# Optimization experiments

Hardware: AMD Instinct MI355X
Metric: run time of the kernel (lower is better)

Reference implementation:

```python
import jax, jax.numpy as jnp
import numpy as np

NUM_HEADS = 8          # from init_kwargs
MASK_VALUE = -1e6      # torch code sets masked scores to -1e6 (not -inf)


def setup_inputs() -> dict:
    key = jax.random.key(0)
    k1, k2, k3, k4, k5 = jax.random.split(key, 5)
    n, S, d = 256, 512, 128   # n = B(2) * num_windows(16) * num_heads(8)
    W = 16                    # num_windows
    return {
        "queries": jax.random.normal(k1, (n, S, d), jnp.float32),
        "keys": jax.random.normal(k2, (n, S, d), jnp.float32),
        "values": jax.random.normal(k3, (n, S, d), jnp.float32),
        "valid_lens": jax.random.randint(k4, (n,), 0, S, jnp.int32),
        "window_mask": jax.random.normal(k5, (W, S, S), jnp.float32),
    }


def reference(queries, keys, values, valid_lens, window_mask):
    n, Q, d = queries.shape
    Wn, _, K = window_mask.shape
    # scaled QK^T: [n, Q, K]
    scores = jnp.einsum('bqd,bkd->bqk', queries, keys) / jnp.sqrt(
        jnp.asarray(d, queries.dtype))
    # additive window mask, broadcast over (batch, heads)
    B = n // (Wn * NUM_HEADS)
    scores = scores.reshape(B, Wn, NUM_HEADS, Q, K) + window_mask[None, :, None]
    scores = scores.reshape(n, Q, K)
    # valid-length masking: positions >= valid_lens[b] set to -1e6 before softmax
    mask = jnp.arange(K)[None, None, :] < valid_lens[:, None, None]  # [n,1,K]
    scores = jnp.where(mask, scores, MASK_VALUE)
    attn = jax.nn.softmax(scores, axis=-1)
    # dropout p=0.0 (eval) -> identity
    return jnp.einsum('bqk,bkd->bqd', attn, values)
```

## Files before the change

### kernel.cpp

```cpp
#include <hip/hip_runtime.h>

typedef unsigned short u16;
using bf16x8 = __attribute__((ext_vector_type(8))) short;
using f32x4  = __attribute__((ext_vector_type(4))) float;
using s16x4  = __attribute__((ext_vector_type(4))) short;

#define S_LEN 512
#define D_DIM 128
#define CB    32
#define KS    136
#define VS    36
#define KBUF  (CB * KS)
#define VBUF  (D_DIM * VS)
#define SCALE 0.08838834764831845f

__device__ __forceinline__ unsigned int cvt_pk_bf16(float lo, float hi) {
  unsigned int r;
  asm("v_cvt_pk_bf16_f32 %0, %1, %2" : "=v"(r) : "v"(lo), "v"(hi));
  return r;
}
__device__ __forceinline__ bf16x8 pack8(f32x4 a, f32x4 b) {
  union { unsigned int u[4]; bf16x8 v; } r;
  r.u[0] = cvt_pk_bf16(a[0], a[1]);
  r.u[1] = cvt_pk_bf16(a[2], a[3]);
  r.u[2] = cvt_pk_bf16(b[0], b[1]);
  r.u[3] = cvt_pk_bf16(b[2], b[3]);
  return r.v;
}

__global__ __launch_bounds__(256, 3)
void attn_fused(const float* __restrict__ Q, const float* __restrict__ K,
                const float* __restrict__ V, const int* __restrict__ VL,
                const float* __restrict__ WM, float* __restrict__ O) {
  __shared__ short smem[2 * KBUF + 2 * VBUF];

  const int bid  = blockIdx.x;
  const int n    = (bid & 7) | ((bid >> 6) << 3);
  const int qt   = (bid >> 3) & 7;
  const int tid  = threadIdx.x;
  const int wave = tid >> 6;
  const int L    = tid & 63;
  const int quad = L >> 4;
  const int lq   = L & 15;
  const int qw   = qt * 64 + wave * 16;
  const int qg   = qw + lq;
  const int w    = (n >> 3) & 15;

  short* Ksh = smem;
  short* VTb = smem + 2 * KBUF;

  const float* Qn  = Q + (size_t)n * S_LEN * D_DIM;
  const float* Kn  = K + (size_t)n * S_LEN * D_DIM;
  const float* Vn  = V + (size_t)n * S_LEN * D_DIM;
  const float* WMq = WM + ((size_t)w * S_LEN + qg) * S_LEN;

  const int vlen  = VL[n];
  const int kvlim = (vlen == 0) ? S_LEN : vlen;
  const int nch   = (kvlim + CB - 1) / CB;

  bf16x8 qf[4];
#pragma unroll
  for (int dc = 0; dc < 4; ++dc) {
    const f32x4* qp = (const f32x4*)(Qn + (size_t)qg * D_DIM + dc * 32 + quad * 8);
    qf[dc] = pack8(qp[0], qp[1]);
  }

  f32x4 o[8];
#pragma unroll
  for (int t = 0; t < 8; ++t) o[t] = (f32x4){0.f, 0.f, 0.f, 0.f};
  float mrun = -1e30f, lrun = 0.f;

  const int tr = tid >> 4;
  const int cc = tid & 15;
  const int colsw = (cc & 7) << 2;
  const float* Kst = Kn + (size_t)tr * D_DIM + cc * 8;
  const float* Vst = Vn + (size_t)tr * D_DIM + cc * 8;

  f32x4 k0a, k0b, k1a, k1b, v0a, v0b, v1a, v1b;

#define STAGE_ISSUE(cb_) {                                              \
    const float* kp0 = Kst + (size_t)(cb_) * D_DIM;                     \
    const float* kp1 = kp0 + 16 * D_DIM;                                \
    const float* vp0 = Vst + (size_t)(cb_) * D_DIM;                     \
    const float* vp1 = vp0 + 16 * D_DIM;                                \
    k0a = ((const f32x4*)kp0)[0]; k0b = ((const f32x4*)kp0)[1];         \
    k1a = ((const f32x4*)kp1)[0]; k1b = ((const f32x4*)kp1)[1];         \
    v0a = ((const f32x4*)vp0)[0]; v0b = ((const f32x4*)vp0)[1];         \
    v1a = ((const f32x4*)vp1)[0]; v1b = ((const f32x4*)vp1)[1]; }

#define STAGE_WRITE(kd, vd) {                                           \
    *(bf16x8*)((kd) + tr * KS + cc * 8)        = pack8(k0a, k0b);       \
    *(bf16x8*)((kd) + (16 + tr) * KS + cc * 8) = pack8(k1a, k1b);       \
    short* vt0 = (vd) + (cc * 8) * VS + (tr ^ colsw);                   \
    short* vt1 = (vd) + (cc * 8) * VS + ((16 + tr) ^ colsw);            \
    unsigned int wa0 = cvt_pk_bf16(v0a[0], v0a[1]);                     \
    unsigned int wa1 = cvt_pk_bf16(v0a[2], v0a[3]);                     \
    unsigned int wa2 = cvt_pk_bf16(v0b[0], v0b[1]);                     \
    unsigned int wa3 = cvt_pk_bf16(v0b[2], v0b[3]);                     \
    vt0[0 * VS] = (short)(wa0);  vt0[1 * VS] = (short)(wa0 >> 16);      \
    vt0[2 * VS] = (short)(wa1);  vt0[3 * VS] = (short)(wa1 >> 16);      \
    vt0[4 * VS] = (short)(wa2);  vt0[5 * VS] = (short)(wa2 >> 16);      \
    vt0[6 * VS] = (short)(wa3);  vt0[7 * VS] = (short)(wa3 >> 16);      \
    unsigned int wb0 = cvt_pk_bf16(v1a[0], v1a[1]);                     \
    unsigned int wb1 = cvt_pk_bf16(v1a[2], v1a[3]);                     \
    unsigned int wb2 = cvt_pk_bf16(v1b[0], v1b[1]);                     \
    unsigned int wb3 = cvt_pk_bf16(v1b[2], v1b[3]);                     \
    vt1[0 * VS] = (short)(wb0);  vt1[1 * VS] = (short)(wb0 >> 16);      \
    vt1[2 * VS] = (short)(wb1);  vt1[3 * VS] = (short)(wb1 >> 16);      \
    vt1[4 * VS] = (short)(wb2);  vt1[5 * VS] = (short)(wb2 >> 16);      \
    vt1[6 * VS] = (short)(wb3);  vt1[7 * VS] = (short)(wb3 >> 16); }

  STAGE_ISSUE(0);
  STAGE_WRITE(Ksh, VTb);
  asm volatile("s_waitcnt lgkmcnt(0)" ::: "memory");
  __builtin_amdgcn_s_barrier();

  int buf = 0;
  for (int ci = 0; ci < nch; ++ci) {
    const int cb   = ci * CB;
    const int cpre = (ci + 1 < nch ? ci + 1 : nch - 1) * CB;

    STAGE_ISSUE(cpre);
    f32x4 wm0 = *(const f32x4*)(WMq + cb + quad * 4);
    f32x4 wm1 = *(const f32x4*)(WMq + cb + 16 + quad * 4);
    __builtin_amdgcn_sched_barrier(0);

    const short* Kc = Ksh + buf * KBUF;
    const short* Vc = VTb + buf * VBUF;

    f32x4 a0 = {0, 0, 0, 0}, a1 = {0, 0, 0, 0};
#pragma unroll
    for (int dc = 0; dc < 4; ++dc) {
      bf16x8 kf0 = *(const bf16x8*)(Kc + lq * KS + dc * 32 + quad * 8);
      bf16x8 kf1 = *(const bf16x8*)(Kc + (16 + lq) * KS + dc * 32 + quad * 8);
      a0 = __builtin_amdgcn_mfma_f32_16x16x32_bf16(kf0, qf[dc], a0, 0, 0, 0);
      a1 = __builtin_amdgcn_mfma_f32_16x16x32_bf16(kf1, qf[dc], a1, 0, 0, 0);
    }
    float s0[4], s1[4];
    float mloc = -1e30f;
#pragma unroll
    for (int r = 0; r < 4; ++r) {
      int k0i = cb + quad * 4 + r;
      s0[r] = (k0i < vlen)      ? a0[r] * SCALE + wm0[r] : -1e6f;
      s1[r] = (k0i + 16 < vlen) ? a1[r] * SCALE + wm1[r] : -1e6f;
      mloc = fmaxf(mloc, fmaxf(s0[r], s1[r]));
    }
    mloc = fmaxf(mloc, __shfl_xor(mloc, 16, 64));
    mloc = fmaxf(mloc, __shfl_xor(mloc, 32, 64));
    const float mnew  = fmaxf(mrun, mloc);
    const float alpha = __expf(mrun - mnew);
    mrun = mnew;

    float ev[8];
#pragma unroll
    for (int r = 0; r < 4; ++r) {
      ev[r]     = __expf(s0[r] - mnew);
      ev[4 + r] = __expf(s1[r] - mnew);
    }
    union { unsigned int u[4]; bf16x8 v; } pfu;
    pfu.u[0] = cvt_pk_bf16(ev[0], ev[1]);
    pfu.u[1] = cvt_pk_bf16(ev[2], ev[3]);
    pfu.u[2] = cvt_pk_bf16(ev[4], ev[5]);
    pfu.u[3] = cvt_pk_bf16(ev[6], ev[7]);
    float psum = 0.f;
#pragma unroll
    for (int t2 = 0; t2 < 4; ++t2) {
      union { unsigned int i; float f; } lo, hi;
      lo.i = pfu.u[t2] << 16;
      hi.i = pfu.u[t2] & 0xffff0000u;
      psum += lo.f + hi.f;
    }
    psum += __shfl_xor(psum, 16, 64);
    psum += __shfl_xor(psum, 32, 64);
    lrun = lrun * alpha + psum;

    float ar[4];
#pragma unroll
    for (int r = 0; r < 4; ++r) ar[r] = __shfl(alpha, quad * 4 + r, 64);

    const bf16x8 pf = pfu.v;

#pragma unroll
    for (int t = 0; t < 8; ++t) {
      int d   = 16 * t + lq;
      int swz = ((d >> 3) & 7) << 2;
      s16x4 b0 = *(const s16x4*)(Vc + d * VS + ((quad * 4) ^ swz));
      s16x4 b1 = *(const s16x4*)(Vc + d * VS + ((16 + quad * 4) ^ swz));
      bf16x8 bv = {b0[0], b0[1], b0[2], b0[3], b1[0], b1[1], b1[2], b1[3]};
      f32x4 ot = o[t];
#pragma unroll
      for (int r = 0; r < 4; ++r) ot[r] *= ar[r];
      o[t] = __builtin_amdgcn_mfma_f32_16x16x32_bf16(pf, bv, ot, 0, 0, 0);
    }

    __builtin_amdgcn_sched_barrier(0);
    STAGE_WRITE(Ksh + (buf ^ 1) * KBUF, VTb + (buf ^ 1) * VBUF);
    asm volatile("s_waitcnt lgkmcnt(0)" ::: "memory");
    __builtin_amdgcn_s_barrier();
    buf ^= 1;
  }

  float linv[4];
#pragma unroll
  for (int r = 0; r < 4; ++r) {
    float lr = __shfl(lrun, quad * 4 + r, 64);
    linv[r] = 1.f / lr;
  }
  float* ow = (float*)smem + wave * (16 * 132);
#pragma unroll
  for (int t = 0; t < 8; ++t) {
#pragma unroll
    for (int r = 0; r < 4; ++r) {
      ow[(quad * 4 + r) * 132 + 16 * t + lq] = o[t][r] * linv[r];
    }
  }
  asm volatile("s_waitcnt lgkmcnt(0)" ::: "memory");
  float* On = O + (size_t)n * S_LEN * D_DIM;
  const int half = L >> 5;
  const int c4   = (L & 31) * 4;
#pragma unroll
  for (int p = 0; p < 8; ++p) {
    int row = 2 * p + half;
    f32x4 v = *(const f32x4*)(ow + row * 132 + c4);
    *(f32x4*)(On + (size_t)(qw + row) * D_DIM + c4) = v;
  }
}

extern "C" void kernel_launch(void* const* d_in, const int* in_sizes, int n_in,
                              void* d_out, int out_size, void* d_ws, size_t ws_size,
                              hipStream_t stream) {
  const float* Q  = (const float*)d_in[0];
  const float* K  = (const float*)d_in[1];
  const float* V  = (const float*)d_in[2];
  const int*   VL = (const int*)d_in[3];
  const float* WM = (const float*)d_in[4];
  float* O = (float*)d_out;
  dim3 grid(256 * 8), block(256);
  attn_fused<<<grid, block, 0, stream>>>(Q, K, V, VL, WM, O);
}
```

Measured before the change: 253.2 us.

## Deepen K/V global prefetch to two chunks ahead with dual register sets

Adds a second register set for staged K/V global loads so that loads are issued two chunks ahead instead of one. The loop is unrolled by two with fixed LDS buffers, alternating the A and B register sets. This hides more global memory latency per chunk. In exchange it raises VGPR pressure by 32 floats per thread, which may hurt occupancy under launch_bounds(256,3) or cause spills.

```diff
diff --git a/kernel.cpp b/kernel.cpp
--- a/kernel.cpp
+++ b/kernel.cpp
@@ -46,8 +46,10 @@
   const int qg   = qw + lq;
   const int w    = (n >> 3) & 15;
 
-  short* Ksh = smem;
-  short* VTb = smem + 2 * KBUF;
+  short* K0 = smem;
+  short* K1 = smem + KBUF;
+  short* V0 = smem + 2 * KBUF;
+  short* V1 = V0 + VBUF;
 
   const float* Qn  = Q + (size_t)n * S_LEN * D_DIM;
   const float* Kn  = K + (size_t)n * S_LEN * D_DIM;
@@ -57,6 +59,7 @@
   const int vlen  = VL[n];
   const int kvlim = (vlen == 0) ? S_LEN : vlen;
   const int nch   = (kvlim + CB - 1) / CB;
+  const int nchm1 = nch - 1;
 
   bf16x8 qf[4];
 #pragma unroll
@@ -76,57 +79,44 @@
   const float* Kst = Kn + (size_t)tr * D_DIM + cc * 8;
   const float* Vst = Vn + (size_t)tr * D_DIM + cc * 8;
 
-  f32x4 k0a, k0b, k1a, k1b, v0a, v0b, v1a, v1b;
-
-#define STAGE_ISSUE(cb_) {                                              \
+  f32x4 Ak0a, Ak0b, Ak1a, Ak1b, Av0a, Av0b, Av1a, Av1b;
+  f32x4 Bk0a, Bk0b, Bk1a, Bk1b, Bv0a, Bv0b, Bv1a, Bv1b;
+
+#define STAGE_ISSUE(P, cb_) {                                           \
     const float* kp0 = Kst + (size_t)(cb_) * D_DIM;                     \
     const float* kp1 = kp0 + 16 * D_DIM;                                \
     const float* vp0 = Vst + (size_t)(cb_) * D_DIM;                     \
     const float* vp1 = vp0 + 16 * D_DIM;                                \
-    k0a = ((const f32x4*)kp0)[0]; k0b = ((const f32x4*)kp0)[1];         \
-    k1a = ((const f32x4*)kp1)[0]; k1b = ((const f32x4*)kp1)[1];         \
-    v0a = ((const f32x4*)vp0)[0]; v0b = ((const f32x4*)vp0)[1];         \
-    v1a = ((const f32x4*)vp1)[0]; v1b = ((const f32x4*)vp1)[1]; }
-
-#define STAGE_WRITE(kd, vd) {                                           \
-    *(bf16x8*)((kd) + tr * KS + cc * 8)        = pack8(k0a, k0b);       \
-    *(bf16x8*)((kd) + (16 + tr) * KS + cc * 8) = pack8(k1a, k1b);       \
+    P##k0a = ((const f32x4*)kp0)[0]; P##k0b = ((const f32x4*)kp0)[1];   \
+    P##k1a = ((const f32x4*)kp1)[0]; P##k1b = ((const f32x4*)kp1)[1];   \
+    P##v0a = ((const f32x4*)vp0)[0]; P##v0b = ((const f32x4*)vp0)[1];   \
+    P##v1a = ((const f32x4*)vp1)[0]; P##v1b = ((const f32x4*)vp1)[1]; }
+
+#define STAGE_WRITE(P, kd, vd) {                                        \
+    *(bf16x8*)((kd) + tr * KS + cc * 8)        = pack8(P##k0a, P##k0b); \
+    *(bf16x8*)((kd) + (16 + tr) * KS + cc * 8) = pack8(P##k1a, P##k1b); \
     short* vt0 = (vd) + (cc * 8) * VS + (tr ^ colsw);                   \
     short* vt1 = (vd) + (cc * 8) * VS + ((16 + tr) ^ colsw);            \
-    unsigned int wa0 = cvt_pk_bf16(v0a[0], v0a[1]);                     \
-    unsigned int wa1 = cvt_pk_bf16(v0a[2], v0a[3]);                     \
-    unsigned int wa2 = cvt_pk_bf16(v0b[0], v0b[1]);                     \
-    unsigned int wa3 = cvt_pk_bf16(v0b[2], v0b[3]);                     \
+    unsigned int wa0 = cvt_pk_bf16(P##v0a[0], P##v0a[1]);               \
+    unsigned int wa1 = cvt_pk_bf16(P##v0a[2], P##v0a[3]);               \
+    unsigned int wa2 = cvt_pk_bf16(P##v0b[0], P##v0b[1]);               \
+    unsigned int wa3 = cvt_pk_bf16(P##v0b[2], P##v0b[3]);               \
     vt0[0 * VS] = (short)(wa0);  vt0[1 * VS] = (short)(wa0 >> 16);      \
     vt0[2 * VS] = (short)(wa1);  vt0[3 * VS] = (short)(wa1 >> 16);      \
     vt0[4 * VS] = (short)(wa2);  vt0[5 * VS] = (short)(wa2 >> 16);      \
     vt0[6 * VS] = (short)(wa3);  vt0[7 * VS] = (short)(wa3 >> 16);      \
-    unsigned int wb0 = cvt_pk_bf16(v1a[0], v1a[1]);                     \
-    unsigned int wb1 = cvt_pk_bf16(v1a[2], v1a[3]);                     \
-    unsigned int wb2 = cvt_pk_bf16(v1b[0], v1b[1]);                     \
-    unsigned int wb3 = cvt_pk_bf16(v1b[2], v1b[3]);                     \
+    unsigned int wb0 = cvt_pk_bf16(P##v1a[0], P##v1a[1]);               \
+    unsigned int wb1 = cvt_pk_bf16(P##v1a[2], P##v1a[3]);               \
+    unsigned int wb2 = cvt_pk_bf16(P##v1b[0], P##v1b[1]);               \
+    unsigned int wb3 = cvt_pk_bf16(P##v1b[2], P##v1b[3]);               \
     vt1[0 * VS] = (short)(wb0);  vt1[1 * VS] = (short)(wb0 >> 16);      \
     vt1[2 * VS] = (short)(wb1);  vt1[3 * VS] = (short)(wb1 >> 16);      \
     vt1[4 * VS] = (short)(wb2);  vt1[5 * VS] = (short)(wb2 >> 16);      \
     vt1[6 * VS] = (short)(wb3);  vt1[7 * VS] = (short)(wb3 >> 16); }
 
-  STAGE_ISSUE(0);
-  STAGE_WRITE(Ksh, VTb);
-  asm volatile("s_waitcnt lgkmcnt(0)" ::: "memory");
-  __builtin_amdgcn_s_barrier();
-
-  int buf = 0;
-  for (int ci = 0; ci < nch; ++ci) {
-    const int cb   = ci * CB;
-    const int cpre = (ci + 1 < nch ? ci + 1 : nch - 1) * CB;
-
-    STAGE_ISSUE(cpre);
+  auto compute_chunk = [&](int cb, const short* Kc, const short* Vc) {
     f32x4 wm0 = *(const f32x4*)(WMq + cb + quad * 4);
     f32x4 wm1 = *(const f32x4*)(WMq + cb + 16 + quad * 4);
-    __builtin_amdgcn_sched_barrier(0);
-
-    const short* Kc = Ksh + buf * KBUF;
-    const short* Vc = VTb + buf * VBUF;
 
     f32x4 a0 = {0, 0, 0, 0}, a1 = {0, 0, 0, 0};
 #pragma unroll
@@ -179,7 +169,6 @@
     for (int r = 0; r < 4; ++r) ar[r] = __shfl(alpha, quad * 4 + r, 64);
 
     const bf16x8 pf = pfu.v;
-
 #pragma unroll
     for (int t = 0; t < 8; ++t) {
       int d   = 16 * t + lq;
@@ -192,13 +181,46 @@
       for (int r = 0; r < 4; ++r) ot[r] *= ar[r];
       o[t] = __builtin_amdgcn_mfma_f32_16x16x32_bf16(pf, bv, ot, 0, 0, 0);
     }
-
-    __builtin_amdgcn_sched_barrier(0);
-    STAGE_WRITE(Ksh + (buf ^ 1) * KBUF, VTb + (buf ^ 1) * VBUF);
-    asm volatile("s_waitcnt lgkmcnt(0)" ::: "memory");
-    __builtin_amdgcn_s_barrier();
-    buf ^= 1;
-  }
+  };
+
+  STAGE_ISSUE(A, 0);
+  {
+    const int c1 = (1 <= nchm1 ? 1 : nchm1) * CB;
+    STAGE_ISSUE(B, c1);
+  }
+  STAGE_WRITE(A, K0, V0);
+  asm volatile("s_waitcnt lgkmcnt(0)" ::: "memory");
+  __builtin_amdgcn_s_barrier();
+
+  int ci = 0;
+  for (;;) {
+    {
+      const int cp = (ci + 2 <= nchm1 ? ci + 2 : nchm1) * CB;
+      STAGE_ISSUE(A, cp);
+      __builtin_amdgcn_sched_barrier(0);
+      compute_chunk(ci * CB, K0, V0);
+      if (ci + 1 >= nch) break;
+      __builtin_amdgcn_sched_barrier(0);
+      STAGE_WRITE(B, K1, V1);
+      asm volatile("s_waitcnt lgkmcnt(0)" ::: "memory");
+      __builtin_amdgcn_s_barrier();
+    }
+    {
+      const int cp = (ci + 3 <= nchm1 ? ci + 3 : nchm1) * CB;
+      STAGE_ISSUE(B, cp);
+      __builtin_amdgcn_sched_barrier(0);
+      compute_chunk((ci + 1) * CB, K1, V1);
+      if (ci + 2 >= nch) break;
+      __builtin_amdgcn_sched_barrier(0);
+      STAGE_WRITE(A, K0, V0);
+      asm volatile("s_waitcnt lgkmcnt(0)" ::: "memory");
+      __builtin_amdgcn_s_barrier();
+    }
+    ci += 2;
+  }
+
+  asm volatile("s_waitcnt lgkmcnt(0)" ::: "memory");
+  __builtin_amdgcn_s_barrier();
 
   float linv[4];
 #pragma unroll
```

New measurement: 247.7 us. 1.02x faster.

## Single-buffer K/V LDS staging and raise occupancy to four blocks per CU

Applied to the files above, without the earlier changes.

Replaces the double-buffered K/V shared-memory tiles with a single buffer, using register prefetch plus two barriers per chunk. This halves LDS use, and launch bounds are raised from 3 to 4 blocks per SM so more blocks fit. The epilogue is split into two 64-column halves so the output staging fits in the smaller LDS. In exchange, each chunk pays an extra barrier, loses overlap between LDS writes and compute, and the compiler has a tighter register budget.

```diff
diff --git a/kernel.cpp b/kernel.cpp
--- a/kernel.cpp
+++ b/kernel.cpp
@@ -12,6 +12,7 @@
 #define VS    36
 #define KBUF  (CB * KS)
 #define VBUF  (D_DIM * VS)
+#define OWS   68
 #define SCALE 0.08838834764831845f
 
 __device__ __forceinline__ unsigned int cvt_pk_bf16(float lo, float hi) {
@@ -28,11 +29,11 @@
   return r.v;
 }
 
-__global__ __launch_bounds__(256, 3)
+__global__ __launch_bounds__(256, 4)
 void attn_fused(const float* __restrict__ Q, const float* __restrict__ K,
                 const float* __restrict__ V, const int* __restrict__ VL,
                 const float* __restrict__ WM, float* __restrict__ O) {
-  __shared__ short smem[2 * KBUF + 2 * VBUF];
+  __shared__ short smem[KBUF + VBUF];
 
   const int bid  = blockIdx.x;
   const int n    = (bid & 7) | ((bid >> 6) << 3);
@@ -47,7 +48,7 @@
   const int w    = (n >> 3) & 15;
 
   short* Ksh = smem;
-  short* VTb = smem + 2 * KBUF;
+  short* VTs = smem + KBUF;
 
   const float* Qn  = Q + (size_t)n * S_LEN * D_DIM;
   const float* Kn  = K + (size_t)n * S_LEN * D_DIM;
@@ -57,6 +58,7 @@
   const int vlen  = VL[n];
   const int kvlim = (vlen == 0) ? S_LEN : vlen;
   const int nch   = (kvlim + CB - 1) / CB;
+  const int nchm1 = nch - 1;
 
   bf16x8 qf[4];
 #pragma unroll
@@ -76,63 +78,49 @@
   const float* Kst = Kn + (size_t)tr * D_DIM + cc * 8;
   const float* Vst = Vn + (size_t)tr * D_DIM + cc * 8;
 
-  f32x4 k0a, k0b, k1a, k1b, v0a, v0b, v1a, v1b;
+  f32x4 Ak0a, Ak0b, Ak1a, Ak1b, Av0a, Av0b, Av1a, Av1b;
 
 #define STAGE_ISSUE(cb_) {                                              \
     const float* kp0 = Kst + (size_t)(cb_) * D_DIM;                     \
     const float* kp1 = kp0 + 16 * D_DIM;                                \
     const float* vp0 = Vst + (size_t)(cb_) * D_DIM;                     \
     const float* vp1 = vp0 + 16 * D_DIM;                                \
-    k0a = ((const f32x4*)kp0)[0]; k0b = ((const f32x4*)kp0)[1];         \
-    k1a = ((const f32x4*)kp1)[0]; k1b = ((const f32x4*)kp1)[1];         \
-    v0a = ((const f32x4*)vp0)[0]; v0b = ((const f32x4*)vp0)[1];         \
-    v1a = ((const f32x4*)vp1)[0]; v1b = ((const f32x4*)vp1)[1]; }
-
-#define STAGE_WRITE(kd, vd) {                                           \
-    *(bf16x8*)((kd) + tr * KS + cc * 8)        = pack8(k0a, k0b);       \
-    *(bf16x8*)((kd) + (16 + tr) * KS + cc * 8) = pack8(k1a, k1b);       \
-    short* vt0 = (vd) + (cc * 8) * VS + (tr ^ colsw);                   \
-    short* vt1 = (vd) + (cc * 8) * VS + ((16 + tr) ^ colsw);            \
-    unsigned int wa0 = cvt_pk_bf16(v0a[0], v0a[1]);                     \
-    unsigned int wa1 = cvt_pk_bf16(v0a[2], v0a[3]);                     \
-    unsigned int wa2 = cvt_pk_bf16(v0b[0], v0b[1]);                     \
-    unsigned int wa3 = cvt_pk_bf16(v0b[2], v0b[3]);                     \
+    Ak0a = ((const f32x4*)kp0)[0]; Ak0b = ((const f32x4*)kp0)[1];       \
+    Ak1a = ((const f32x4*)kp1)[0]; Ak1b = ((const f32x4*)kp1)[1];       \
+    Av0a = ((const f32x4*)vp0)[0]; Av0b = ((const f32x4*)vp0)[1];       \
+    Av1a = ((const f32x4*)vp1)[0]; Av1b = ((const f32x4*)vp1)[1]; }
+
+#define STAGE_WRITE() {                                                 \
+    *(bf16x8*)(Ksh + tr * KS + cc * 8)        = pack8(Ak0a, Ak0b);      \
+    *(bf16x8*)(Ksh + (16 + tr) * KS + cc * 8) = pack8(Ak1a, Ak1b);      \
+    short* vt0 = VTs + (cc * 8) * VS + (tr ^ colsw);                    \
+    short* vt1 = VTs + (cc * 8) * VS + ((16 + tr) ^ colsw);             \
+    unsigned int wa0 = cvt_pk_bf16(Av0a[0], Av0a[1]);                   \
+    unsigned int wa1 = cvt_pk_bf16(Av0a[2], Av0a[3]);                   \
+    unsigned int wa2 = cvt_pk_bf16(Av0b[0], Av0b[1]);                   \
+    unsigned int wa3 = cvt_pk_bf16(Av0b[2], Av0b[3]);                   \
     vt0[0 * VS] = (short)(wa0);  vt0[1 * VS] = (short)(wa0 >> 16);      \
     vt0[2 * VS] = (short)(wa1);  vt0[3 * VS] = (short)(wa1 >> 16);      \
     vt0[4 * VS] = (short)(wa2);  vt0[5 * VS] = (short)(wa2 >> 16);      \
     vt0[6 * VS] = (short)(wa3);  vt0[7 * VS] = (short)(wa3 >> 16);      \
-    unsigned int wb0 = cvt_pk_bf16(v1a[0], v1a[1]);                     \
-    unsigned int wb1 = cvt_pk_bf16(v1a[2], v1a[3]);                     \
-    unsigned int wb2 = cvt_pk_bf16(v1b[0], v1b[1]);                     \
-    unsigned int wb3 = cvt_pk_bf16(v1b[2], v1b[3]);                     \
+    unsigned int wb0 = cvt_pk_bf16(Av1a[0], Av1a[1]);                   \
+    unsigned int wb1 = cvt_pk_bf16(Av1a[2], Av1a[3]);                   \
+    unsigned int wb2 = cvt_pk_bf16(Av1b[0], Av1b[1]);                   \
+    unsigned int wb3 = cvt_pk_bf16(Av1b[2], Av1b[3]);                   \
     vt1[0 * VS] = (short)(wb0);  vt1[1 * VS] = (short)(wb0 >> 16);      \
     vt1[2 * VS] = (short)(wb1);  vt1[3 * VS] = (short)(wb1 >> 16);      \
     vt1[4 * VS] = (short)(wb2);  vt1[5 * VS] = (short)(wb2 >> 16);      \
     vt1[6 * VS] = (short)(wb3);  vt1[7 * VS] = (short)(wb3 >> 16); }
 
-  STAGE_ISSUE(0);
-  STAGE_WRITE(Ksh, VTb);
-  asm volatile("s_waitcnt lgkmcnt(0)" ::: "memory");
-  __builtin_amdgcn_s_barrier();
-
-  int buf = 0;
-  for (int ci = 0; ci < nch; ++ci) {
-    const int cb   = ci * CB;
-    const int cpre = (ci + 1 < nch ? ci + 1 : nch - 1) * CB;
-
-    STAGE_ISSUE(cpre);
+  auto compute_chunk = [&](int cb) {
     f32x4 wm0 = *(const f32x4*)(WMq + cb + quad * 4);
     f32x4 wm1 = *(const f32x4*)(WMq + cb + 16 + quad * 4);
-    __builtin_amdgcn_sched_barrier(0);
-
-    const short* Kc = Ksh + buf * KBUF;
-    const short* Vc = VTb + buf * VBUF;
 
     f32x4 a0 = {0, 0, 0, 0}, a1 = {0, 0, 0, 0};
 #pragma unroll
     for (int dc = 0; dc < 4; ++dc) {
-      bf16x8 kf0 = *(const bf16x8*)(Kc + lq * KS + dc * 32 + quad * 8);
-      bf16x8 kf1 = *(const bf16x8*)(Kc + (16 + lq) * KS + dc * 32 + quad * 8);
+      bf16x8 kf0 = *(const bf16x8*)(Ksh + lq * KS + dc * 32 + quad * 8);
+      bf16x8 kf1 = *(const bf16x8*)(Ksh + (16 + lq) * KS + dc * 32 + quad * 8);
       a0 = __builtin_amdgcn_mfma_f32_16x16x32_bf16(kf0, qf[dc], a0, 0, 0, 0);
       a1 = __builtin_amdgcn_mfma_f32_16x16x32_bf16(kf1, qf[dc], a1, 0, 0, 0);
     }
@@ -179,26 +167,34 @@
     for (int r = 0; r < 4; ++r) ar[r] = __shfl(alpha, quad * 4 + r, 64);
 
     const bf16x8 pf = pfu.v;
-
 #pragma unroll
     for (int t = 0; t < 8; ++t) {
       int d   = 16 * t + lq;
       int swz = ((d >> 3) & 7) << 2;
-      s16x4 b0 = *(const s16x4*)(Vc + d * VS + ((quad * 4) ^ swz));
-      s16x4 b1 = *(const s16x4*)(Vc + d * VS + ((16 + quad * 4) ^ swz));
+      s16x4 b0 = *(const s16x4*)(VTs + d * VS + ((quad * 4) ^ swz));
+      s16x4 b1 = *(const s16x4*)(VTs + d * VS + ((16 + quad * 4) ^ swz));
       bf16x8 bv = {b0[0], b0[1], b0[2], b0[3], b1[0], b1[1], b1[2], b1[3]};
       f32x4 ot = o[t];
 #pragma unroll
       for (int r = 0; r < 4; ++r) ot[r] *= ar[r];
       o[t] = __builtin_amdgcn_mfma_f32_16x16x32_bf16(pf, bv, ot, 0, 0, 0);
     }
-
-    __builtin_amdgcn_sched_barrier(0);
-    STAGE_WRITE(Ksh + (buf ^ 1) * KBUF, VTb + (buf ^ 1) * VBUF);
-    asm volatile("s_waitcnt lgkmcnt(0)" ::: "memory");
-    __builtin_amdgcn_s_barrier();
-    buf ^= 1;
-  }
+  };
+
+  STAGE_ISSUE(0);
+  STAGE_WRITE();
+  __syncthreads();
+
+  for (int ci = 0;;) {
+    const int cpre = (ci + 1 <= nchm1 ? ci + 1 : nchm1) * CB;
+    STAGE_ISSUE(cpre);
+    compute_chunk(ci * CB);
+    if (++ci >= nch) break;
+    __syncthreads();
+    STAGE_WRITE();
+    __syncthreads();
+  }
+  __syncthreads();
 
   float linv[4];
 #pragma unroll
@@ -206,23 +202,24 @@
     float lr = __shfl(lrun, quad * 4 + r, 64);
     linv[r] = 1.f / lr;
   }
-  float* ow = (float*)smem + wave * (16 * 132);
-#pragma unroll
-  for (int t = 0; t < 8; ++t) {
-#pragma unroll
-    for (int r = 0; r < 4; ++r) {
-      ow[(quad * 4 + r) * 132 + 16 * t + lq] = o[t][r] * linv[r];
-    }
-  }
-  asm volatile("s_waitcnt lgkmcnt(0)" ::: "memory");
+  float* ow = (float*)smem + wave * (16 * OWS);
   float* On = O + (size_t)n * S_LEN * D_DIM;
-  const int half = L >> 5;
-  const int c4   = (L & 31) * 4;
-#pragma unroll
-  for (int p = 0; p < 8; ++p) {
-    int row = 2 * p + half;
-    f32x4 v = *(const f32x4*)(ow + row * 132 + c4);
-    *(f32x4*)(On + (size_t)(qw + row) * D_DIM + c4) = v;
+  const int row = L >> 2;
+  const int cb4 = (L & 3) * 16;
+#pragma unroll
+  for (int h = 0; h < 2; ++h) {
+#pragma unroll
+    for (int tt = 0; tt < 4; ++tt) {
+      const int t = h * 4 + tt;
+#pragma unroll
+      for (int r = 0; r < 4; ++r)
+        ow[(quad * 4 + r) * OWS + tt * 16 + lq] = o[t][r] * linv[r];
+    }
+#pragma unroll
+    for (int j = 0; j < 4; ++j) {
+      f32x4 v = *(const f32x4*)(ow + row * OWS + cb4 + 4 * j);
+      *(f32x4*)(On + (size_t)(qw + row) * D_DIM + h * 64 + cb4 + 4 * j) = v;
+    }
   }
 }
 
```

Measured after the change: 254.5 us. No clear change (+0.5%).
